# Optimization experiments

Hardware: AMD Instinct MI355X
Metric: run time of the kernel (lower is better)

The kernel has to match this reference:

```python
import jax, jax.numpy as jnp
import numpy as np

B, T, H, UNITS = 64, 2048, 512, 512


def setup_inputs() -> dict:
    key = jax.random.key(0)
    ks = jax.random.split(key, 9)
    s = 0.02
    return {
        "query": jax.random.normal(ks[0], (B, H), jnp.float32),
        "cellstate": jax.random.normal(ks[1], (B, H), jnp.float32),
        "values": jax.random.normal(ks[2], (B, T, H), jnp.float32),
        "W1": jax.random.normal(ks[3], (2 * H, UNITS), jnp.float32) * s,
        "b1": jnp.zeros((UNITS,), jnp.float32),
        "W2": jax.random.normal(ks[4], (H, UNITS), jnp.float32) * s,
        "b2": jnp.zeros((UNITS,), jnp.float32),
        "V": jax.random.normal(ks[5], (UNITS, 1), jnp.float32) * s,
        "bv": jnp.zeros((1,), jnp.float32),
    }


def reference(query, cellstate, values, W1, b1, W2, b2, V, bv):
    # query, cellstate: [B, H]; values: [B, T, H]
    qc = jnp.concatenate([query, cellstate], axis=-1)        # [B, 2H]
    proj_q = qc @ W1 + b1                                    # [B, units]
    proj_v = jnp.einsum("bth,hu->btu", values, W2) + b2      # [B, T, units]
    feat = jnp.tanh(proj_q[:, None, :] + proj_v)             # [B, T, units]
    score = jnp.einsum("btu,uo->bto", feat, V) + bv          # [B, T, 1]
    attention_weights = jax.nn.softmax(score, axis=1)        # [B, T, 1]
    context_vector = jnp.sum(attention_weights * values, axis=1)  # [B, H]
    return context_vector, attention_weights
```

## Files before the change

### kernel.cpp

```cpp
#include <hip/hip_runtime.h>
#include <stdint.h>

#define B_ 64
#define T_ 2048
#define H_ 512
#define U_ 512
#define BT 128
#define BK 32
#define BKPW 20

typedef short bf16x8 __attribute__((ext_vector_type(8)));
typedef float f32x4 __attribute__((ext_vector_type(4)));

static __device__ __forceinline__ uint32_t f2bf(float f) {
  uint32_t u = __float_as_uint(f);
  return (u + 0x7fffu + ((u >> 16) & 1u)) >> 16;
}
static __device__ __forceinline__ uint32_t pack2(float lo, float hi) {
  return f2bf(lo) | (f2bf(hi) << 16);
}
static __device__ __forceinline__ float fast_tanh(float x) {
  float z = fminf(fmaxf(x, -15.f), 15.f);
  float e = __expf(2.f * z);
  return (e - 1.f) / (e + 1.f);
}

__global__ void k_proj(const float* __restrict__ q, const float* __restrict__ c,
                       const float* __restrict__ W1, const float* __restrict__ b1,
                       const float* __restrict__ b2, float* __restrict__ P) {
  int u = (blockIdx.x & 1) * 256 + threadIdx.x;
  int b = blockIdx.x >> 1;
  const float* qr = q + b * H_;
  const float* cr = c + b * H_;
  float acc = 0.f;
  for (int k = 0; k < H_; ++k) acc = fmaf(qr[k], W1[k * U_ + u], acc);
  for (int k = 0; k < H_; ++k) acc = fmaf(cr[k], W1[(H_ + k) * U_ + u], acc);
  P[b * U_ + u] = acc + b1[u] + b2[u];
}

__global__ void k_w2t(const float* __restrict__ W2, uint16_t* __restrict__ W2t) {
  int lin = blockIdx.x * 256 + threadIdx.x;
  int u = lin >> 9, k = lin & 511;
  W2t[u * 512 + k] = (uint16_t)f2bf(W2[k * 512 + u]);
}

__global__ __launch_bounds__(512) void k_scores(
    const float* __restrict__ values, const uint16_t* __restrict__ W2t,
    const float* __restrict__ P, const float* __restrict__ Vw,
    const float* __restrict__ bv, float* __restrict__ scores) {

  __shared__ uint32_t ldsA[BT * BKPW];
  __shared__ uint32_t ldsB[U_ * BKPW];
  __shared__ float Pb[U_];
  __shared__ float Vb[U_];
  __shared__ float ssc[4][BT];

  const int tid = threadIdx.x;
  const int b = blockIdx.y;
  const int t0 = blockIdx.x * BT;
  const int lane = tid & 63;
  const int wid = tid >> 6;
  const int wm = wid >> 2;
  const int wn = wid & 3;
  const int l15 = lane & 15;
  const int l4 = lane >> 4;

  Pb[tid & 511] = P[b * U_ + (tid & 511)];
  Vb[tid & 511] = Vw[tid & 511];

  f32x4 acc[4][8];
#pragma unroll
  for (int mt = 0; mt < 4; ++mt)
#pragma unroll
    for (int nt = 0; nt < 8; ++nt) acc[mt][nt] = (f32x4){0.f, 0.f, 0.f, 0.f};

  const float* Abase = values + ((size_t)b * T_ + t0) * H_;
  const uint32_t* Bsrc = (const uint32_t*)W2t;

  for (int k0 = 0; k0 < H_; k0 += BK) {
    __syncthreads();
    {
      int p = tid;
#pragma unroll
      for (int it = 0; it < 4; ++it, p += 512) {
        int t = p >> 4, kp = p & 15;
        const float2 v = *(const float2*)(Abase + t * H_ + k0 + kp * 2);
        ldsA[t * BKPW + kp] = pack2(v.x, v.y);
      }
      p = tid;
#pragma unroll
      for (int it = 0; it < 16; ++it, p += 512) {
        int u = p >> 4, kp = p & 15;
        ldsB[u * BKPW + kp] = Bsrc[u * (H_ / 2) + (k0 >> 1) + kp];
      }
    }
    __syncthreads();

    bf16x8 afr[4];
    const uint32_t* pa = &ldsA[(wm * 64 + l15) * BKPW + l4 * 4];
#pragma unroll
    for (int mt = 0; mt < 4; ++mt)
      afr[mt] = *(const bf16x8*)(pa + mt * 16 * BKPW);
    const uint32_t* pbp = &ldsB[(wn * 128 + l15) * BKPW + l4 * 4];
#pragma unroll
    for (int nt = 0; nt < 8; ++nt) {
      bf16x8 bfr = *(const bf16x8*)(pbp + nt * 16 * BKPW);
#pragma unroll
      for (int mt = 0; mt < 4; ++mt)
        acc[mt][nt] = __builtin_amdgcn_mfma_f32_16x16x32_bf16(afr[mt], bfr, acc[mt][nt], 0, 0, 0);
    }
  }

  float spart[4][4];
#pragma unroll
  for (int mt = 0; mt < 4; ++mt)
#pragma unroll
    for (int r = 0; r < 4; ++r) spart[mt][r] = 0.f;

#pragma unroll
  for (int nt = 0; nt < 8; ++nt) {
    int u = wn * 128 + nt * 16 + l15;
    float pv = Pb[u], vv = Vb[u];
#pragma unroll
    for (int mt = 0; mt < 4; ++mt) {
#pragma unroll
      for (int r = 0; r < 4; ++r)
        spart[mt][r] += fast_tanh(pv + acc[mt][nt][r]) * vv;
    }
  }
#pragma unroll
  for (int d = 1; d < 16; d <<= 1) {
#pragma unroll
    for (int mt = 0; mt < 4; ++mt)
#pragma unroll
      for (int r = 0; r < 4; ++r)
        spart[mt][r] += __shfl_xor(spart[mt][r], d);
  }
  if (l15 == 0) {
#pragma unroll
    for (int mt = 0; mt < 4; ++mt)
#pragma unroll
      for (int r = 0; r < 4; ++r)
        ssc[wn][wm * 64 + mt * 16 + l4 * 4 + r] = spart[mt][r];
  }
  __syncthreads();
  if (tid < BT) {
    float s = ssc[0][tid] + ssc[1][tid] + ssc[2][tid] + ssc[3][tid] + bv[0];
    scores[(size_t)b * T_ + t0 + tid] = s;
  }
}

__global__ void k_softmax(float* __restrict__ w) {
  __shared__ float red[4];
  __shared__ float red2[4];
  int b = blockIdx.x, tid = threadIdx.x;
  int lane = tid & 63, wid = tid >> 6;
  float* s = w + (size_t)b * T_;
  float v[8];
  float m = -1e30f;
#pragma unroll
  for (int j = 0; j < 8; ++j) { v[j] = s[tid + j * 256]; m = fmaxf(m, v[j]); }
#pragma unroll
  for (int d = 1; d < 64; d <<= 1) m = fmaxf(m, __shfl_xor(m, d));
  if (lane == 0) red[wid] = m;
  __syncthreads();
  m = fmaxf(fmaxf(red[0], red[1]), fmaxf(red[2], red[3]));
  float e[8];
  float sum = 0.f;
#pragma unroll
  for (int j = 0; j < 8; ++j) { e[j] = __expf(v[j] - m); sum += e[j]; }
#pragma unroll
  for (int d = 1; d < 64; d <<= 1) sum += __shfl_xor(sum, d);
  if (lane == 0) red2[wid] = sum;
  __syncthreads();
  sum = red2[0] + red2[1] + red2[2] + red2[3];
  float inv = 1.f / sum;
#pragma unroll
  for (int j = 0; j < 8; ++j) s[tid + j * 256] = e[j] * inv;
}

__global__ void k_context(const float* __restrict__ values, const float* __restrict__ w,
                          float* __restrict__ ctx) {
  int b = blockIdx.z;
  int h = blockIdx.y * 256 + threadIdx.x;
  int t0 = blockIdx.x * 128;
  const float* wb = w + (size_t)b * T_ + t0;
  const float* vb = values + ((size_t)b * T_ + t0) * H_ + h;
  float acc = 0.f;
#pragma unroll 4
  for (int t = 0; t < 128; ++t) acc = fmaf(wb[t], vb[(size_t)t * H_], acc);
  atomicAdd(&ctx[b * H_ + h], acc);
}

extern "C" void kernel_launch(void* const* d_in, const int* in_sizes, int n_in,
                              void* d_out, int out_size, void* d_ws, size_t ws_size,
                              hipStream_t stream) {
  const float* query = (const float*)d_in[0];
  const float* cell  = (const float*)d_in[1];
  const float* values = (const float*)d_in[2];
  const float* W1 = (const float*)d_in[3];
  const float* b1 = (const float*)d_in[4];
  const float* W2 = (const float*)d_in[5];
  const float* b2 = (const float*)d_in[6];
  const float* Vw = (const float*)d_in[7];
  const float* bv = (const float*)d_in[8];

  float* out = (float*)d_out;
  float* wgt = out + B_ * H_;

  char* ws = (char*)d_ws;
  float* P = (float*)ws;
  uint16_t* W2t = (uint16_t*)(ws + 131072);

  hipMemsetAsync(out, 0, B_ * H_ * sizeof(float), stream);
  k_proj<<<128, 256, 0, stream>>>(query, cell, W1, b1, b2, P);
  k_w2t<<<1024, 256, 0, stream>>>(W2, W2t);
  k_scores<<<dim3(T_ / BT, B_), 512, 0, stream>>>(values, W2t, P, Vw, bv, wgt);
  k_softmax<<<B_, 256, 0, stream>>>(wgt);
  k_context<<<dim3(T_ / 128, H_ / 256, B_), 256, 0, stream>>>(values, wgt, out);
}
```

Baseline: 596.6 us.

## Double-buffer score GEMM with direct global-to-LDS loads and MFMA-ready weight layout

```diff
diff --git a/kernel.cpp b/kernel.cpp
--- a/kernel.cpp
+++ b/kernel.cpp
@@ -7,7 +7,7 @@
 #define U_ 512
 #define BT 128
 #define BK 32
-#define BKPW 20
+#define KT 16
 
 typedef short bf16x8 __attribute__((ext_vector_type(8)));
 typedef float f32x4 __attribute__((ext_vector_type(4)));
@@ -38,19 +38,24 @@
   P[b * U_ + u] = acc + b1[u] + b2[u];
 }
 
-__global__ void k_w2t(const float* __restrict__ W2, uint16_t* __restrict__ W2t) {
+__global__ void k_w2b(const float* __restrict__ W2, uint32_t* __restrict__ wsB) {
   int lin = blockIdx.x * 256 + threadIdx.x;
-  int u = lin >> 9, k = lin & 511;
-  W2t[u * 512 + k] = (uint16_t)f2bf(W2[k * 512 + u]);
-}
-
-__global__ __launch_bounds__(512) void k_scores(
-    const float* __restrict__ values, const uint16_t* __restrict__ W2t,
+  int u = lin & 511, cg = lin >> 9;
+  int k = cg * 8;
+  uint32_t w0 = pack2(W2[(k + 0) * U_ + u], W2[(k + 1) * U_ + u]);
+  uint32_t w1 = pack2(W2[(k + 2) * U_ + u], W2[(k + 3) * U_ + u]);
+  uint32_t w2 = pack2(W2[(k + 4) * U_ + u], W2[(k + 5) * U_ + u]);
+  uint32_t w3 = pack2(W2[(k + 6) * U_ + u], W2[(k + 7) * U_ + u]);
+  *(uint4*)(wsB + (size_t)lin * 4) = make_uint4(w0, w1, w2, w3);
+}
+
+__global__ __launch_bounds__(512, 2) void k_scores(
+    const float* __restrict__ values, const uint32_t* __restrict__ wsB,
     const float* __restrict__ P, const float* __restrict__ Vw,
-    const float* __restrict__ bv, float* __restrict__ scores) {
-
-  __shared__ uint32_t ldsA[BT * BKPW];
-  __shared__ uint32_t ldsB[U_ * BKPW];
+    float* __restrict__ scores) {
+
+  __shared__ uint32_t lA[2][2048];
+  __shared__ uint32_t lB[2][8192];
   __shared__ float Pb[U_];
   __shared__ float Vb[U_];
   __shared__ float ssc[4][BT];
@@ -65,8 +70,12 @@
   const int l15 = lane & 15;
   const int l4 = lane >> 4;
 
-  Pb[tid & 511] = P[b * U_ + (tid & 511)];
-  Vb[tid & 511] = Vw[tid & 511];
+  Pb[tid] = P[b * U_ + tid];
+  Vb[tid] = Vw[tid];
+
+  const float* Abase = values + ((size_t)b * T_ + t0) * H_;
+  const int sa_t = tid & 127;
+  const int sa_kg = tid >> 7;
 
   f32x4 acc[4][8];
 #pragma unroll
@@ -74,41 +83,49 @@
 #pragma unroll
     for (int nt = 0; nt < 8; ++nt) acc[mt][nt] = (f32x4){0.f, 0.f, 0.f, 0.f};
 
-  const float* Abase = values + ((size_t)b * T_ + t0) * H_;
-  const uint32_t* Bsrc = (const uint32_t*)W2t;
-
-  for (int k0 = 0; k0 < H_; k0 += BK) {
-    __syncthreads();
-    {
-      int p = tid;
-#pragma unroll
-      for (int it = 0; it < 4; ++it, p += 512) {
-        int t = p >> 4, kp = p & 15;
-        const float2 v = *(const float2*)(Abase + t * H_ + k0 + kp * 2);
-        ldsA[t * BKPW + kp] = pack2(v.x, v.y);
-      }
-      p = tid;
-#pragma unroll
-      for (int it = 0; it < 16; ++it, p += 512) {
-        int u = p >> 4, kp = p & 15;
-        ldsB[u * BKPW + kp] = Bsrc[u * (H_ / 2) + (k0 >> 1) + kp];
-      }
+  {
+#pragma unroll
+    for (int i = 0; i < 4; ++i)
+      __builtin_amdgcn_global_load_lds(wsB + i * 2048 + tid * 4,
+                                       &lB[0][i * 2048 + tid * 4], 16, 0, 0);
+    const float4* ap = (const float4*)(Abase + (size_t)sa_t * H_ + sa_kg * 8);
+    float4 x = ap[0], y = ap[1];
+    *(uint4*)&lA[0][sa_kg * 512 + sa_t * 4] =
+        make_uint4(pack2(x.x, x.y), pack2(x.z, x.w), pack2(y.x, y.y), pack2(y.z, y.w));
+  }
+  __syncthreads();
+
+  int buf = 0;
+  for (int kt = 0; kt < KT; ++kt) {
+    const int nb = buf ^ 1;
+    float4 x, y;
+    if (kt < KT - 1) {
+      const int kn = kt + 1;
+      const float4* ap = (const float4*)(Abase + (size_t)sa_t * H_ + kn * BK + sa_kg * 8);
+      x = ap[0]; y = ap[1];
+      const uint32_t* bsrc = wsB + (size_t)kn * 8192;
+#pragma unroll
+      for (int i = 0; i < 4; ++i)
+        __builtin_amdgcn_global_load_lds(bsrc + i * 2048 + tid * 4,
+                                         &lB[nb][i * 2048 + tid * 4], 16, 0, 0);
     }
-    __syncthreads();
-
     bf16x8 afr[4];
-    const uint32_t* pa = &ldsA[(wm * 64 + l15) * BKPW + l4 * 4];
-#pragma unroll
-    for (int mt = 0; mt < 4; ++mt)
-      afr[mt] = *(const bf16x8*)(pa + mt * 16 * BKPW);
-    const uint32_t* pbp = &ldsB[(wn * 128 + l15) * BKPW + l4 * 4];
+#pragma unroll
+    for (int mt = 0; mt < 4; ++mt)
+      afr[mt] = *(const bf16x8*)&lA[buf][l4 * 512 + (wm * 64 + mt * 16 + l15) * 4];
 #pragma unroll
     for (int nt = 0; nt < 8; ++nt) {
-      bf16x8 bfr = *(const bf16x8*)(pbp + nt * 16 * BKPW);
+      bf16x8 bfr = *(const bf16x8*)&lB[buf][l4 * 2048 + (wn * 128 + nt * 16 + l15) * 4];
 #pragma unroll
       for (int mt = 0; mt < 4; ++mt)
         acc[mt][nt] = __builtin_amdgcn_mfma_f32_16x16x32_bf16(afr[mt], bfr, acc[mt][nt], 0, 0, 0);
     }
+    if (kt < KT - 1) {
+      *(uint4*)&lA[nb][sa_kg * 512 + sa_t * 4] =
+          make_uint4(pack2(x.x, x.y), pack2(x.z, x.w), pack2(y.x, y.y), pack2(y.z, y.w));
+    }
+    __syncthreads();
+    buf = nb;
   }
 
   float spart[4][4];
@@ -122,20 +139,19 @@
     int u = wn * 128 + nt * 16 + l15;
     float pv = Pb[u], vv = Vb[u];
 #pragma unroll
-    for (int mt = 0; mt < 4; ++mt) {
+    for (int mt = 0; mt < 4; ++mt)
 #pragma unroll
       for (int r = 0; r < 4; ++r)
         spart[mt][r] += fast_tanh(pv + acc[mt][nt][r]) * vv;
-    }
-  }
-#pragma unroll
-  for (int d = 1; d < 16; d <<= 1) {
+  }
+#pragma unroll
+  for (int d = 1; d < 16; d <<= 1)
 #pragma unroll
     for (int mt = 0; mt < 4; ++mt)
 #pragma unroll
       for (int r = 0; r < 4; ++r)
         spart[mt][r] += __shfl_xor(spart[mt][r], d);
-  }
+
   if (l15 == 0) {
 #pragma unroll
     for (int mt = 0; mt < 4; ++mt)
@@ -145,7 +161,7 @@
   }
   __syncthreads();
   if (tid < BT) {
-    float s = ssc[0][tid] + ssc[1][tid] + ssc[2][tid] + ssc[3][tid] + bv[0];
+    float s = ssc[0][tid] + ssc[1][tid] + ssc[2][tid] + ssc[3][tid];
     scores[(size_t)b * T_ + t0 + tid] = s;
   }
 }
@@ -179,17 +195,24 @@
   for (int j = 0; j < 8; ++j) s[tid + j * 256] = e[j] * inv;
 }
 
-__global__ void k_context(const float* __restrict__ values, const float* __restrict__ w,
-                          float* __restrict__ ctx) {
-  int b = blockIdx.z;
-  int h = blockIdx.y * 256 + threadIdx.x;
+__global__ __launch_bounds__(256) void k_context(const float* __restrict__ values,
+                                                 const float* __restrict__ w,
+                                                 float* __restrict__ ctx) {
+  int b = blockIdx.y;
   int t0 = blockIdx.x * 128;
+  int tid = threadIdx.x;
   const float* wb = w + (size_t)b * T_ + t0;
-  const float* vb = values + ((size_t)b * T_ + t0) * H_ + h;
-  float acc = 0.f;
-#pragma unroll 4
-  for (int t = 0; t < 128; ++t) acc = fmaf(wb[t], vb[(size_t)t * H_], acc);
-  atomicAdd(&ctx[b * H_ + h], acc);
+  const float2* vb = (const float2*)(values + ((size_t)b * T_ + t0) * H_) + tid;
+  float ax = 0.f, ay = 0.f;
+#pragma unroll 8
+  for (int t = 0; t < 128; ++t) {
+    float ww = wb[t];
+    float2 v = vb[(size_t)t * 256];
+    ax = fmaf(ww, v.x, ax);
+    ay = fmaf(ww, v.y, ay);
+  }
+  atomicAdd(&ctx[b * H_ + tid * 2], ax);
+  atomicAdd(&ctx[b * H_ + tid * 2 + 1], ay);
 }
 
 extern "C" void kernel_launch(void* const* d_in, const int* in_sizes, int n_in,
@@ -203,19 +226,18 @@
   const float* W2 = (const float*)d_in[5];
   const float* b2 = (const float*)d_in[6];
   const float* Vw = (const float*)d_in[7];
-  const float* bv = (const float*)d_in[8];
 
   float* out = (float*)d_out;
   float* wgt = out + B_ * H_;
 
   char* ws = (char*)d_ws;
   float* P = (float*)ws;
-  uint16_t* W2t = (uint16_t*)(ws + 131072);
+  uint32_t* wsB = (uint32_t*)(ws + 131072);
 
   hipMemsetAsync(out, 0, B_ * H_ * sizeof(float), stream);
   k_proj<<<128, 256, 0, stream>>>(query, cell, W1, b1, b2, P);
-  k_w2t<<<1024, 256, 0, stream>>>(W2, W2t);
-  k_scores<<<dim3(T_ / BT, B_), 512, 0, stream>>>(values, W2t, P, Vw, bv, wgt);
+  k_w2b<<<128, 256, 0, stream>>>(W2, wsB);
+  k_scores<<<dim3(T_ / BT, B_), 512, 0, stream>>>(values, wsB, P, Vw, wgt);
   k_softmax<<<B_, 256, 0, stream>>>(wgt);
-  k_context<<<dim3(T_ / 128, H_ / 256, B_), 256, 0, stream>>>(values, wgt, out);
-}
+  k_context<<<dim3(T_ / 128, B_), 256, 0, stream>>>(values, wgt, out);
+}
```

Result: faster. 539.4 us (-9.6%).
